# Optimization experiments

Measured on AMD Instinct MI355X. Metric: run time of the kernel, lower is better.

Reference implementation:

```python
import jax, jax.numpy as jnp
import numpy as np

B, T, N, F, CH = 64, 8, 2000, 16, 64  # batch, timesteps(=receptive field), nodes, in features, channels (h_dim//2)
TASK = CH          # task_dim = h_dim // 2
P_TREAT = 0.5      # args.p
P1 = 1.0           # args.p1
BN_EPS = 1e-5


def setup_inputs() -> dict:
    key = jax.random.key(0)
    ks = jax.random.split(key, 40)
    def rn(i, shape, s=0.1):
        return jax.random.normal(ks[i], shape, dtype=jnp.float32) * s
    return {
        "X": jax.random.normal(ks[0], (B, T, N, F), dtype=jnp.float32),
        "A": jax.random.uniform(ks[1], (N, N), dtype=jnp.float32),
        "C": jax.random.randint(ks[2], (B, N), 0, 2, dtype=jnp.int32),
        "Y": jax.random.uniform(ks[3], (B, N), dtype=jnp.float32),
        "Cc": jnp.zeros((B, N), jnp.float32),
        "start_w": rn(4, (CH, F)),
        "start_b": rn(5, (CH,), 0.01),
        "filt_w": rn(6, (3, CH, CH, 2)),
        "filt_b": rn(7, (3, CH), 0.01),
        "gate_w": rn(8, (3, CH, CH, 2)),
        "gate_b": rn(9, (3, CH), 0.01),
        "skip_w": rn(10, (3, CH, CH)),
        "skip_b": rn(11, (3, CH), 0.01),
        "bn_g": 1.0 + rn(12, (3, CH), 0.01),
        "bn_b": rn(13, (3, CH), 0.01),
        "nodevec1": jax.random.normal(ks[14], (N, 10), dtype=jnp.float32),
        "nodevec2": jax.random.normal(ks[15], (10, N), dtype=jnp.float32),
        "task_emb": rn(16, (TASK,)),
        "gcn_w": rn(17, (CH, 3 * CH)),
        "gcn_b": rn(18, (CH,), 0.01),
        "h0_w1": rn(19, (CH, TASK + CH)),
        "h0_b1": rn(20, (CH,), 0.01),
        "h0_w2": rn(21, (1, CH)),
        "h0_b2": rn(22, (1,), 0.01),
        "h1_w1": rn(23, (CH, TASK + CH)),
        "h1_b1": rn(24, (CH,), 0.01),
        "h1_w2": rn(25, (1, CH)),
        "h1_b2": rn(26, (1,), 0.01),
    }


def _conv1x1(x, w, b):
    # x: (B,Cin,N,L), w: (Cout,Cin)
    return jnp.einsum('bcnl,oc->bonl', x, w) + b[None, :, None, None]


def _dil_conv(x, w, b, d):
    # kernel (1,2), dilation d along time, no padding -> width shrinks by d
    L = x.shape[-1]
    y = (jnp.einsum('bcnl,oc->bonl', x[..., :L - d], w[:, :, 0])
         + jnp.einsum('bcnl,oc->bonl', x[..., d:], w[:, :, 1]))
    return y + b[None, :, None, None]


def reference(X, A, C, Y, Cc, start_w, start_b, filt_w, filt_b, gate_w, gate_b,
              skip_w, skip_b, bn_g, bn_b, nodevec1, nodevec2, task_emb, gcn_w, gcn_b,
              h0_w1, h0_b1, h0_w2, h0_b2, h1_w1, h1_b1, h1_w2, h1_b2):
    x = jnp.transpose(X, (0, 3, 2, 1))            # (B,F,N,T)
    x = _conv1x1(x, start_w, start_b)             # (B,CH,N,T)
    adp = jax.nn.softmax(jax.nn.relu(nodevec1 @ nodevec2), axis=1)  # (N,N)
    skip = None
    d = 1
    for i in range(3):  # layers, dilations 1,2,4
        res = x
        f = jnp.tanh(_dil_conv(res, filt_w[i], filt_b[i], d))
        g = jax.nn.sigmoid(_dil_conv(res, gate_w[i], gate_b[i], d))
        x = f * g
        s = _conv1x1(x, skip_w[i], skip_b[i])
        skip = s if skip is None else s + skip[..., -s.shape[-1]:]
        x = x + res[..., -x.shape[-1]:]
        # eval-mode BatchNorm2d with running_mean=0, running_var=1
        scale = (bn_g[i] / jnp.sqrt(1.0 + BN_EPS))[None, :, None, None]
        x = x * scale + bn_b[i][None, :, None, None]
        d *= 2
    # gcn on skip (width 1): out = [x, A@x, A@(A@x)] -> concat -> 1x1 (dropout=eval identity)
    x1 = jnp.einsum('bcvl,vw->bcwl', skip, adp)
    x2 = jnp.einsum('bcvl,vw->bcwl', x1, adp)
    h = jnp.concatenate([skip, x1, x2], axis=1)   # (B,3CH,N,1)
    gx = jax.nn.relu(_conv1x1(h, gcn_w, gcn_b))   # (B,CH,N,1)
    bs, _, n_nodes, _ = gx.shape
    task = jnp.broadcast_to(task_emb[None, :, None, None], (bs, TASK, n_nodes, 1))
    z = jnp.concatenate([task, gx], axis=1)       # (B,TASK+CH,N,1)

    def hyp(w1, b1, w2, b2):
        hh = jax.nn.relu(_conv1x1(z, w1, b1))
        return _conv1x1(hh, w2, b2).reshape(-1)

    y1 = jax.nn.sigmoid(hyp(h1_w1, h1_b1, h1_w2, h1_b2))
    y0 = jax.nn.sigmoid(hyp(h0_w1, h0_b1, h0_w2, h0_b2))
    t = C.reshape(-1)
    y = jnp.where(t > 0, y1, y0)
    yc = jnp.clip(y, 1e-7, 1.0 - 1e-7)
    Yf = Y.reshape(-1)
    bce = -jnp.mean(Yf * jnp.log(yc) + (1.0 - Yf) * jnp.log(1.0 - yc))
    # linear MMD (mmd2_lin, CFR): masked means, jit-friendly
    zb = jnp.transpose(z, (0, 2, 1, 3)).reshape(bs * n_nodes, -1)  # (B*N, TASK+CH)
    tm = (t > 0).astype(zb.dtype)
    mean_t = (tm @ zb) / jnp.maximum(tm.sum(), 1.0)
    mean_c = ((1.0 - tm) @ zb) / jnp.maximum((1.0 - tm).sum(), 1.0)
    imb = jnp.sum((2.0 * P_TREAT * mean_t - 2.0 * (1.0 - P_TREAT) * mean_c) ** 2)
    loss = bce + P1 * imb
    return (loss, y, y0, y1)
```

## Files before the change

kernel.cpp:

```cpp
#include <hip/hip_runtime.h>
#include <cstdint>

#define NB 64
#define TT 8
#define NN 2000
#define NF 16
#define NCH 64
#define NPAD 2048
#define BCD 4096
#define ITEMS 128000

#define OFF_ADPF  0
#define OFF_ST    4194304
#define OFF_X2    0
#define OFF_ADPT  8388608
#define OFF_S     10485760
#define OFF_X1F   18874368
#define OFF_X1T   27262976
#define OFF_C01   31457280
#define OFF_WGCNT (OFF_C01 + 128)
#define OFF_W1TT  (OFF_WGCNT + 12288)
#define OFF_PART  (OFF_W1TT + 8192)
#define OFF_RED   (OFF_PART + 270336)
#define OFF_WAW   (OFF_RED + 136)
#define OFF_SWW   (OFF_WAW + 24576)
#define OFF_WSTW  (OFF_SWW + 6144)

#define SWZK(k, x) (((k) & ~63) | (((((k) >> 3) & 7) ^ ((x) & 7)) << 3) | ((k) & 7))
#define GSWZ(n) ((((n) >> 3) ^ (n)) & 7)

typedef __attribute__((ext_vector_type(8))) short short8;
typedef __attribute__((ext_vector_type(4))) float f32x4;
typedef const __attribute__((address_space(1))) uint32_t* gas_t;
typedef __attribute__((address_space(3))) uint32_t* las_t;

__device__ __forceinline__ float fast_rcp(float x) { return __builtin_amdgcn_rcpf(x); }
__device__ __forceinline__ float fast_tanh(float x) {
    x = fminf(fmaxf(x, -10.f), 10.f);
    float e = __expf(2.f * x);
    return (e - 1.f) * fast_rcp(e + 1.f);
}
__device__ __forceinline__ float fast_sigmoid(float x) {
    return fast_rcp(1.f + __expf(-x));
}
__device__ __forceinline__ unsigned short f2bf(float f) {
    uint32_t u = __float_as_uint(f);
    u += 0x7fff + ((u >> 16) & 1);
    return (unsigned short)(u >> 16);
}
__device__ __forceinline__ float bf2f(unsigned short b) {
    return __uint_as_float(((uint32_t)b) << 16);
}

__global__ __launch_bounds__(256) void prep_kernel(const float* __restrict__ gcn_w,
                            const float* __restrict__ h0_w1, const float* __restrict__ h0_b1,
                            const float* __restrict__ h1_w1, const float* __restrict__ h1_b1,
                            const float* __restrict__ task_emb,
                            const float* __restrict__ filt_w, const float* __restrict__ gate_w,
                            const float* __restrict__ skip_w, const float* __restrict__ start_w,
                            float* __restrict__ c01, float* __restrict__ wgcnT,
                            float* __restrict__ w1tT,
                            unsigned short* __restrict__ waw,
                            unsigned short* __restrict__ sww,
                            unsigned short* __restrict__ wstw)
{
    const int GS = 64 * 256;
    int gt = blockIdx.x * 256 + threadIdx.x;
    for (int idx = gt; idx < 64 * 192; idx += GS) {
        int o = idx / 192, j = idx % 192;
        wgcnT[j * 64 + o] = gcn_w[idx];
    }
    for (int idx = gt; idx < 4096; idx += GS) {
        int o = idx >> 6, c = idx & 63;
        w1tT[c * 64 + o]        = h0_w1[o * 128 + 64 + c];
        w1tT[4096 + c * 64 + o] = h1_w1[o * 128 + 64 + c];
    }
    for (int job = gt; job < 3 * 2 * 128 * 8; job += GS) {
        int L = job / 2048, rem = job % 2048;
        int p = rem >> 10, rem2 = rem & 1023;
        int r = rem2 >> 3, chp = rem2 & 7;
        int cho = chp ^ (r & 7);
        #pragma unroll
        for (int i = 0; i < 8; ++i) {
            int c = cho * 8 + i;
            float v = (r < 64) ? filt_w[L * 8192 + r * 128 + c * 2 + p]
                               : gate_w[L * 8192 + (r - 64) * 128 + c * 2 + p];
            waw[((L * 2 + p) * 128 + r) * 64 + chp * 8 + i] = f2bf(v);
        }
    }
    for (int job = gt; job < 3 * 64 * 8; job += GS) {
        int L = job / 512, rem = job % 512;
        int r = rem >> 3, chp = rem & 7;
        int cho = chp ^ (r & 7);
        #pragma unroll
        for (int i = 0; i < 8; ++i)
            sww[(L * 64 + r) * 64 + chp * 8 + i] = f2bf(skip_w[L * 4096 + r * 64 + cho * 8 + i]);
    }
    for (int job = gt; job < 64 * 8; job += GS) {
        int r = job >> 3, chp = job & 7;
        int cho = chp ^ (r & 7);
        #pragma unroll
        for (int i = 0; i < 8; ++i) {
            int k = cho * 8 + i;
            wstw[r * 64 + chp * 8 + i] = (k < 16) ? f2bf(start_w[r * 16 + k]) : (unsigned short)0;
        }
    }
    if (gt < 128) {
        int head = gt >> 6, o = gt & 63;
        const float* w1 = head ? h1_w1 : h0_w1;
        const float* b1 = head ? h1_b1 : h0_b1;
        float a = b1[o];
        for (int k = 0; k < 64; ++k) a = fmaf(w1[o * 128 + k], task_emb[k], a);
        c01[gt] = a;
    }
}

__global__ __launch_bounds__(256) void adp_kernel(const float* __restrict__ nv1,
                                                  const float* __restrict__ nv2,
                                                  float* __restrict__ adpF)
{
    __shared__ float nv1s[10];
    __shared__ float rbuf[4];
    int tid = threadIdx.x;
    int r = blockIdx.x;
    if (tid < 10) nv1s[tid] = nv1[r * 10 + tid];
    __syncthreads();

    float val[8];
    float vmax = -3.4e38f;
    #pragma unroll
    for (int s = 0; s < 8; ++s) {
        int j = tid + s * 256;
        if (j < NN) {
            float v = 0.f;
            #pragma unroll
            for (int k = 0; k < 10; ++k) v = fmaf(nv1s[k], nv2[k * NN + j], v);
            v = fmaxf(v, 0.f);
            val[s] = v;
            vmax = fmaxf(vmax, v);
        } else val[s] = -3.4e38f;
    }
    for (int off = 32; off; off >>= 1) vmax = fmaxf(vmax, __shfl_down(vmax, off, 64));
    if ((tid & 63) == 0) rbuf[tid >> 6] = vmax;
    __syncthreads();
    vmax = fmaxf(fmaxf(rbuf[0], rbuf[1]), fmaxf(rbuf[2], rbuf[3]));
    __syncthreads();
    float sum = 0.f;
    #pragma unroll
    for (int s = 0; s < 8; ++s) {
        int j = tid + s * 256;
        if (j < NN) { val[s] = expf(val[s] - vmax); sum += val[s]; }
    }
    for (int off = 32; off; off >>= 1) sum += __shfl_down(sum, off, 64);
    if ((tid & 63) == 0) rbuf[tid >> 6] = sum;
    __syncthreads();
    sum = rbuf[0] + rbuf[1] + rbuf[2] + rbuf[3];
    float inv = 1.f / sum;
    #pragma unroll
    for (int s = 0; s < 8; ++s) {
        int j = tid + s * 256;
        if (j < NN) adpF[(size_t)r * NPAD + j] = val[s] * inv;
    }
}

__global__ __launch_bounds__(256) void transpose_adp(const float* __restrict__ adpF,
                                                     unsigned short* __restrict__ adpT)
{
    __shared__ float tile[64][65];
    int tid = threadIdx.x;
    int r0 = blockIdx.x * 64;
    int j0 = blockIdx.y * 64;
    #pragma unroll
    for (int s = 0; s < 16; ++s) {
        int idx = s * 256 + tid;
        int i = idx >> 6, jj = idx & 63;
        int r = r0 + i, j = j0 + jj;
        tile[i][jj] = (r < NN && j < NN) ? adpF[(size_t)r * NPAD + j] : 0.f;
    }
    __syncthreads();
    #pragma unroll
    for (int s = 0; s < 2; ++s) {
        int slot = s * 256 + tid;
        int j = slot >> 3, ch = slot & 7;
        short8 v;
        #pragma unroll
        for (int e = 0; e < 8; ++e) v[e] = (short)f2bf(tile[ch * 8 + e][j]);
        *(short8*)&adpT[(size_t)(j0 + j) * NPAD + r0 + ((ch ^ (j & 7)) << 3)] = v;
    }
}

template<int NG, int WOUT, int D>
__device__ __forceinline__ void mfma_phaseB(int L,
    const unsigned short* __restrict__ xb, unsigned short* __restrict__ gbuf,
    const unsigned short* __restrict__ WA, const float* __restrict__ biasAll,
    int wave, int lr, int lk)
{
    if (wave >= NG) return;
    int idx = wave * 16 + lr;
    int n = (idx / WOUT) * 8 + (idx % WOUT);
    f32x4 aF[4], aG[4];
    #pragma unroll
    for (int mt = 0; mt < 4; ++mt) {
        aF[mt] = (f32x4){0.f, 0.f, 0.f, 0.f};
        aG[mt] = (f32x4){0.f, 0.f, 0.f, 0.f};
    }
    #pragma unroll
    for (int p = 0; p < 2; ++p) {
        int nb = n + p * D;
        const unsigned short* WAp = WA + p * 8192;
        #pragma unroll
        for (int ks = 0; ks < 2; ++ks) {
            short8 bv = *(const short8*)&xb[(nb * 8 + ((ks * 4 + lk) ^ (nb & 7))) * 8];
            #pragma unroll
            for (int mt = 0; mt < 4; ++mt) {
                int r = mt * 16 + lr;
                short8 av = *(const short8*)&WAp[(r * 8 + ((ks * 4 + lk) ^ (r & 7))) * 8];
                aF[mt] = __builtin_amdgcn_mfma_f32_16x16x32_bf16(av, bv, aF[mt], 0, 0, 0);
            }
            #pragma unroll
            for (int mt = 0; mt < 4; ++mt) {
                int r = (mt + 4) * 16 + lr;
                short8 av = *(const short8*)&WAp[(r * 8 + ((ks * 4 + lk) ^ (r & 7))) * 8];
                aG[mt] = __builtin_amdgcn_mfma_f32_16x16x32_bf16(av, bv, aG[mt], 0, 0, 0);
            }
        }
    }
    int gs = GSWZ(n);
    #pragma unroll
    for (int mt = 0; mt < 4; ++mt) {
        int ob = mt * 16 + lk * 4;
        ushort4 p;
        p.x = f2bf(fast_tanh(aF[mt][0] + biasAll[L * 128 + ob + 0]) * fast_sigmoid(aG[mt][0] + biasAll[L * 128 + 64 + ob + 0]));
        p.y = f2bf(fast_tanh(aF[mt][1] + biasAll[L * 128 + ob + 1]) * fast_sigmoid(aG[mt][1] + biasAll[L * 128 + 64 + ob + 1]));
        p.z = f2bf(fast_tanh(aF[mt][2] + biasAll[L * 128 + ob + 2]) * fast_sigmoid(aG[mt][2] + biasAll[L * 128 + 64 + ob + 2]));
        p.w = f2bf(fast_tanh(aF[mt][3] + biasAll[L * 128 + ob + 3]) * fast_sigmoid(aG[mt][3] + biasAll[L * 128 + 64 + ob + 3]));
        *(ushort4*)&gbuf[((n * 8) + ((mt * 2 + (lk >> 1)) ^ gs)) * 8 + (lk & 1) * 4] = p;
    }
}

template<int L, int D, int WOUT>
__device__ __forceinline__ void phaseC_conv(unsigned short* __restrict__ xb,
    const unsigned short* __restrict__ gbuf,
    const float* __restrict__ bn_g, const float* __restrict__ bn_b,
    float xreg[8], int wave, int o)
{
    float bsc = bn_g[L * 64 + o] * rsqrtf(1.0f + 1e-5f);
    float bsh = bn_b[L * 64 + o];
    int g = wave;
    #pragma unroll
    for (int t = 0; t < WOUT; ++t) {
        int n = g * 8 + t;
        float gv = bf2f(gbuf[(n * 8 + ((o >> 3) ^ GSWZ(n))) * 8 + (o & 7)]);
        float nx = (gv + xreg[t + D]) * bsc + bsh;
        xreg[t] = nx;
        xb[(n * 8 + ((o >> 3) ^ (n & 7))) * 8 + (o & 7)] = f2bf(nx);
    }
}

__device__ __forceinline__ void phaseC_skip(int LASTT,
    const unsigned short* __restrict__ gbuf, const unsigned short* __restrict__ SW,
    f32x4 skacc[4], int wave, int lr, int lk)
{
    if (wave != 0) return;
    int n = lr * 8 + LASTT;
    int gs = GSWZ(n);
    #pragma unroll
    for (int ks = 0; ks < 2; ++ks) {
        short8 bv = *(const short8*)&gbuf[(n * 8 + ((ks * 4 + lk) ^ gs)) * 8];
        #pragma unroll
        for (int mt = 0; mt < 4; ++mt) {
            int r = mt * 16 + lr;
            short8 av = *(const short8*)&SW[(r * 8 + ((ks * 4 + lk) ^ (r & 7))) * 8];
            skacc[mt] = __builtin_amdgcn_mfma_f32_16x16x32_bf16(av, bv, skacc[mt], 0, 0, 0);
        }
    }
}

__global__ __launch_bounds__(1024) void temporal_kernel(
    const float* __restrict__ X,
    const float* __restrict__ start_b,
    const unsigned short* __restrict__ waw,
    const unsigned short* __restrict__ sww,
    const unsigned short* __restrict__ wstw,
    const float* __restrict__ filt_b, const float* __restrict__ gate_b,
    const float* __restrict__ skip_b,
    const float* __restrict__ bn_g, const float* __restrict__ bn_b,
    float* __restrict__ S, unsigned short* __restrict__ St)
{
    extern __shared__ float smem[];
    unsigned short* xb   = (unsigned short*)smem;
    unsigned short* gbuf = (unsigned short*)(smem + 4096);
    unsigned short* WA   = (unsigned short*)(smem + 8192);
    unsigned short* SW   = (unsigned short*)(smem + 16384);
    float* biasAll       = smem + 18432;

    int tid = threadIdx.x;
    int wave = tid >> 6, lane = tid & 63;
    int lr = lane & 15, lk = lane >> 4;
    int o = lane;
    int item0 = blockIdx.x * 16;

    if (tid < 512)
        __builtin_amdgcn_global_load_lds((gas_t)(wstw + tid * 8), (las_t)(WA + tid * 8), 16, 0, 0);
    if (tid < 384) {
        int L = tid >> 7, oo = tid & 127;
        biasAll[tid] = (oo < 64) ? filt_b[L * 64 + oo] : gate_b[L * 64 + oo - 64];
    }
    {
        int n = tid >> 3, c = tid & 7;
        int g = n >> 3, t = n & 7;
        int ig = item0 + g, b = ig / NN, nn = ig - b * NN;
        int cho = c ^ (n & 7);
        short8 v = {0, 0, 0, 0, 0, 0, 0, 0};
        if (cho < 2) {
            const float* src = &X[((size_t)(b * TT + t) * NN + nn) * NF + cho * 8];
            float4 f0 = *(const float4*)src;
            float4 f1 = *(const float4*)(src + 4);
            v[0] = (short)f2bf(f0.x); v[1] = (short)f2bf(f0.y);
            v[2] = (short)f2bf(f0.z); v[3] = (short)f2bf(f0.w);
            v[4] = (short)f2bf(f1.x); v[5] = (short)f2bf(f1.y);
            v[6] = (short)f2bf(f1.z); v[7] = (short)f2bf(f1.w);
        }
        *(short8*)&xb[(n * 8 + c) * 8] = v;
    }
    __syncthreads();

    if (wave < 8) {
        f32x4 aS[4];
        #pragma unroll
        for (int mt = 0; mt < 4; ++mt) aS[mt] = (f32x4){0.f, 0.f, 0.f, 0.f};
        int n = wave * 16 + lr;
        short8 bv = *(const short8*)&xb[(n * 8 + (lk ^ (n & 7))) * 8];
        #pragma unroll
        for (int mt = 0; mt < 4; ++mt) {
            int r = mt * 16 + lr;
            short8 av = *(const short8*)&WA[(r * 8 + (lk ^ (r & 7))) * 8];
            aS[mt] = __builtin_amdgcn_mfma_f32_16x16x32_bf16(av, bv, aS[mt], 0, 0, 0);
        }
        int gs = GSWZ(n);
        #pragma unroll
        for (int mt = 0; mt < 4; ++mt) {
            ushort4 p;
            p.x = f2bf(aS[mt][0]); p.y = f2bf(aS[mt][1]);
            p.z = f2bf(aS[mt][2]); p.w = f2bf(aS[mt][3]);
            *(ushort4*)&gbuf[((n * 8) + ((mt * 2 + (lk >> 1)) ^ gs)) * 8 + (lk & 1) * 4] = p;
        }
    }
    if (tid < 512)
        __builtin_amdgcn_global_load_lds((gas_t)(sww + tid * 8), (las_t)(SW + tid * 8), 16, 0, 0);
    __syncthreads();

    float xreg[8];
    f32x4 skacc[4];
    #pragma unroll
    for (int mt = 0; mt < 4; ++mt) skacc[mt] = (f32x4){0.f, 0.f, 0.f, 0.f};

    {
        __builtin_amdgcn_global_load_lds((gas_t)(waw + (size_t)tid * 8),
                                         (las_t)(WA + tid * 8), 16, 0, 0);
        __builtin_amdgcn_global_load_lds((gas_t)(waw + (size_t)(tid + 1024) * 8),
                                         (las_t)(WA + (tid + 1024) * 8), 16, 0, 0);
        float sb = start_b[o];
        int g = wave;
        #pragma unroll
        for (int t = 0; t < 8; ++t) {
            int n = g * 8 + t;
            float gv = bf2f(gbuf[(n * 8 + ((o >> 3) ^ GSWZ(n))) * 8 + (o & 7)]) + sb;
            xreg[t] = gv;
            xb[(n * 8 + ((o >> 3) ^ (n & 7))) * 8 + (o & 7)] = f2bf(gv);
        }
    }
    __syncthreads();

    mfma_phaseB<7, 7, 1>(0, xb, gbuf, WA, biasAll, wave, lr, lk);
    __syncthreads();
    phaseC_skip(6, gbuf, SW, skacc, wave, lr, lk);
    phaseC_conv<0, 1, 7>(xb, gbuf, bn_g, bn_b, xreg, wave, o);
    __builtin_amdgcn_global_load_lds((gas_t)(waw + (size_t)(16384 + tid * 8)),
                                     (las_t)(WA + tid * 8), 16, 0, 0);
    __builtin_amdgcn_global_load_lds((gas_t)(waw + (size_t)(16384 + (tid + 1024) * 8)),
                                     (las_t)(WA + (tid + 1024) * 8), 16, 0, 0);
    __syncthreads();

    mfma_phaseB<5, 5, 2>(1, xb, gbuf, WA, biasAll, wave, lr, lk);
    if (tid < 512)
        __builtin_amdgcn_global_load_lds((gas_t)(sww + (size_t)(4096 + tid * 8)),
                                         (las_t)(SW + tid * 8), 16, 0, 0);
    __syncthreads();
    phaseC_skip(4, gbuf, SW, skacc, wave, lr, lk);
    phaseC_conv<1, 2, 5>(xb, gbuf, bn_g, bn_b, xreg, wave, o);
    __builtin_amdgcn_global_load_lds((gas_t)(waw + (size_t)(32768 + tid * 8)),
                                     (las_t)(WA + tid * 8), 16, 0, 0);
    __builtin_amdgcn_global_load_lds((gas_t)(waw + (size_t)(32768 + (tid + 1024) * 8)),
                                     (las_t)(WA + (tid + 1024) * 8), 16, 0, 0);
    __syncthreads();

    mfma_phaseB<1, 1, 4>(2, xb, gbuf, WA, biasAll, wave, lr, lk);
    if (tid < 512)
        __builtin_amdgcn_global_load_lds((gas_t)(sww + (size_t)(8192 + tid * 8)),
                                         (las_t)(SW + tid * 8), 16, 0, 0);
    __syncthreads();
    phaseC_skip(0, gbuf, SW, skacc, wave, lr, lk);

    if (wave == 0) {
        int ig = item0 + lr, b = ig / NN, nn = ig - b * NN;
        #pragma unroll
        for (int mt = 0; mt < 4; ++mt) {
            #pragma unroll
            for (int j = 0; j < 4; ++j) {
                int oo = mt * 16 + lk * 4 + j;
                float v = skacc[mt][j] + skip_b[oo] + skip_b[64 + oo] + skip_b[128 + oo];
                int bc = b * 64 + oo;
                S[(size_t)nn * BCD + bc] = v;
                St[(size_t)bc * NPAD + SWZK(nn, oo)] = f2bf(v);
            }
        }
    }
}

__global__ __launch_bounds__(256) void gemm_mfma(
    const unsigned short* __restrict__ A, const unsigned short* __restrict__ B,
    float* __restrict__ Cf, unsigned short* __restrict__ Ct)
{
    __shared__ unsigned short As[128 * 64];
    __shared__ unsigned short Bs[128 * 64];
    int tid = threadIdx.x;
    int wave = tid >> 6, lane = tid & 63;
    int lk = lane >> 4, lr = lane & 15;
    int n0 = blockIdx.x * 128, m0 = blockIdx.y * 128;
    int wm = wave >> 1, wn = wave & 1;

    f32x4 acc[4][4];
    #pragma unroll
    for (int i = 0; i < 4; ++i)
        #pragma unroll
        for (int j = 0; j < 4; ++j)
            acc[i][j] = (f32x4){0.f, 0.f, 0.f, 0.f};

    for (int k0 = 0; k0 < NPAD; k0 += 64) {
        #pragma unroll
        for (int i = 0; i < 4; ++i) {
            int chunk = wave * 4 + i;
            int row = chunk * 8 + (lane >> 3);
            int koff = (lane & 7) * 8;
            __builtin_amdgcn_global_load_lds(
                (gas_t)(A + (size_t)(m0 + row) * NPAD + k0 + koff),
                (las_t)(&As[chunk * 512]), 16, 0, 0);
            __builtin_amdgcn_global_load_lds(
                (gas_t)(B + (size_t)(n0 + row) * NPAD + k0 + koff),
                (las_t)(&Bs[chunk * 512]), 16, 0, 0);
        }
        __syncthreads();
        #pragma unroll
        for (int s = 0; s < 2; ++s) {
            short8 av[4], bv[4];
            #pragma unroll
            for (int f = 0; f < 4; ++f) {
                int m = wm * 64 + f * 16 + lr;
                int ca = ((s * 4 + lk) ^ (m & 7));
                av[f] = *(const short8*)&As[m * 64 + ca * 8];
                int n = wn * 64 + f * 16 + lr;
                int cb = ((s * 4 + lk) ^ (n & 7));
                bv[f] = *(const short8*)&Bs[n * 64 + cb * 8];
            }
            #pragma unroll
            for (int fi = 0; fi < 4; ++fi)
                #pragma unroll
                for (int fj = 0; fj < 4; ++fj)
                    acc[fi][fj] = __builtin_amdgcn_mfma_f32_16x16x32_bf16(
                        av[fi], bv[fj], acc[fi][fj], 0, 0, 0);
        }
        __syncthreads();
    }

    #pragma unroll
    for (int fi = 0; fi < 4; ++fi) {
        #pragma unroll
        for (int fj = 0; fj < 4; ++fj) {
            int m = m0 + wm * 64 + fi * 16 + lk * 4;
            int n = n0 + wn * 64 + fj * 16 + lr;
            f32x4 v = acc[fi][fj];
            if (Cf) {
                Cf[(size_t)(m + 0) * BCD + n] = v[0];
                Cf[(size_t)(m + 1) * BCD + n] = v[1];
                Cf[(size_t)(m + 2) * BCD + n] = v[2];
                Cf[(size_t)(m + 3) * BCD + n] = v[3];
            }
            if (Ct) {
                ushort4 p;
                p.x = f2bf(v[0]); p.y = f2bf(v[1]);
                p.z = f2bf(v[2]); p.w = f2bf(v[3]);
                *(ushort4*)&Ct[(size_t)n * NPAD + SWZK(m, n)] = p;
            }
        }
    }
}

__global__ __launch_bounds__(256) void head_kernel(
    const float* __restrict__ S, const float* __restrict__ x1f,
    const float* __restrict__ x2,
    const float* __restrict__ wgcnT, const float* __restrict__ gcn_b,
    const float* __restrict__ c01, const float* __restrict__ w1tT,
    const float* __restrict__ h0_w2, const float* __restrict__ h0_b2,
    const float* __restrict__ h1_w2, const float* __restrict__ h1_b2,
    const int* __restrict__ Ct, const float* __restrict__ Yf,
    float* __restrict__ out, float* __restrict__ partials)
{
    __shared__ float hl[4][4][192];
    __shared__ float gxl[4][4][64];
    int tid = threadIdx.x;
    int wave = tid >> 6, o = tid & 63;
    int wid = blockIdx.x * 4 + wave;
    float w2a = h0_w2[o], w2b = h1_w2[o];
    float b20 = h0_b2[0], b21 = h1_b2[0];
    float cb = gcn_b[o], c0a = c01[o], c0b = c01[64 + o];

    float accT = 0.f, accC = 0.f, bce = 0.f, cT = 0.f, cC = 0.f;

    for (int base = wid * 4; base < ITEMS; base += 2048 * 4) {
        #pragma unroll
        for (int it = 0; it < 4; ++it) {
            int item = base + it;
            int b = item / NN, n = item - b * NN;
            int bc = b * 64 + o;
            hl[wave][it][o]       = S[(size_t)n * BCD + bc];
            hl[wave][it][64 + o]  = x1f[(size_t)n * BCD + bc];
            hl[wave][it][128 + o] = x2[(size_t)n * BCD + bc];
        }
        float a0 = cb, a1 = cb, a2 = cb, a3 = cb;
        for (int j = 0; j < 192; ++j) {
            float w = wgcnT[j * 64 + o];
            a0 = fmaf(w, hl[wave][0][j], a0);
            a1 = fmaf(w, hl[wave][1][j], a1);
            a2 = fmaf(w, hl[wave][2][j], a2);
            a3 = fmaf(w, hl[wave][3][j], a3);
        }
        float gxv[4] = {fmaxf(a0, 0.f), fmaxf(a1, 0.f), fmaxf(a2, 0.f), fmaxf(a3, 0.f)};
        #pragma unroll
        for (int it = 0; it < 4; ++it) gxl[wave][it][o] = gxv[it];

        float p0[4], p1[4];
        #pragma unroll
        for (int it = 0; it < 4; ++it) { p0[it] = c0a; p1[it] = c0b; }
        for (int c = 0; c < 64; ++c) {
            float w0 = w1tT[c * 64 + o];
            float w1 = w1tT[4096 + c * 64 + o];
            float g0 = gxl[wave][0][c], g1 = gxl[wave][1][c];
            float g2 = gxl[wave][2][c], g3 = gxl[wave][3][c];
            p0[0] = fmaf(w0, g0, p0[0]); p0[1] = fmaf(w0, g1, p0[1]);
            p0[2] = fmaf(w0, g2, p0[2]); p0[3] = fmaf(w0, g3, p0[3]);
            p1[0] = fmaf(w1, g0, p1[0]); p1[1] = fmaf(w1, g1, p1[1]);
            p1[2] = fmaf(w1, g2, p1[2]); p1[3] = fmaf(w1, g3, p1[3]);
        }
        #pragma unroll
        for (int it = 0; it < 4; ++it) {
            float r0 = w2a * fmaxf(p0[it], 0.f);
            float r1 = w2b * fmaxf(p1[it], 0.f);
            #pragma unroll
            for (int off = 32; off; off >>= 1) {
                r0 += __shfl_down(r0, off, 64);
                r1 += __shfl_down(r1, off, 64);
            }
            int item = base + it;
            int tt = Ct[item];
            if (o == 0) {
                float y0 = 1.f / (1.f + expf(-(r0 + b20)));
                float y1 = 1.f / (1.f + expf(-(r1 + b21)));
                float y = (tt > 0) ? y1 : y0;
                out[1 + item] = y;
                out[1 + ITEMS + item] = y0;
                out[1 + 2 * ITEMS + item] = y1;
                float yc = fminf(fmaxf(y, 1e-7f), 1.f - 1e-7f);
                float Yv = Yf[item];
                bce -= Yv * logf(yc) + (1.f - Yv) * logf(1.f - yc);
                if (tt > 0) cT += 1.f; else cC += 1.f;
            }
            if (tt > 0) accT += gxv[it]; else accC += gxv[it];
        }
    }
    partials[wid * 132 + o] = accT;
    partials[wid * 132 + 64 + o] = accC;
    if (o == 0) {
        partials[wid * 132 + 128] = bce;
        partials[wid * 132 + 129] = cT;
        partials[wid * 132 + 130] = cC;
    }
}

__global__ __launch_bounds__(256) void reduce_kernel(const float* __restrict__ partials,
                                                     float* __restrict__ red)
{
    __shared__ float rb[4];
    int slot = blockIdx.x;
    int tid = threadIdx.x;
    float s = 0.f;
    for (int w = tid; w < 2048; w += 256) s += partials[w * 132 + slot];
    #pragma unroll
    for (int off = 32; off; off >>= 1) s += __shfl_down(s, off, 64);
    if ((tid & 63) == 0) rb[tid >> 6] = s;
    __syncthreads();
    if (tid == 0) red[slot] = rb[0] + rb[1] + rb[2] + rb[3];
}

__global__ void final_kernel(const float* __restrict__ red,
                             const float* __restrict__ task_emb,
                             float* __restrict__ out)
{
    int tid = threadIdx.x;
    float cT = red[129], cC = red[130];
    float iT = 1.f / fmaxf(cT, 1.f), iC = 1.f / fmaxf(cC, 1.f);
    float d1 = task_emb[tid] * (cT * iT) - task_emb[tid] * (cC * iC);
    float d2 = red[tid] * iT - red[64 + tid] * iC;
    float p = d1 * d1 + d2 * d2;
    #pragma unroll
    for (int off = 32; off; off >>= 1) p += __shfl_down(p, off, 64);
    if (tid == 0) out[0] = red[128] * (1.f / (float)ITEMS) + p;
}

extern "C" void kernel_launch(void* const* d_in, const int* in_sizes, int n_in,
                              void* d_out, int out_size, void* d_ws, size_t ws_size,
                              hipStream_t stream)
{
    const float* X       = (const float*)d_in[0];
    const int*   Ct      = (const int*)d_in[2];
    const float* Yf      = (const float*)d_in[3];
    const float* start_w = (const float*)d_in[5];
    const float* start_b = (const float*)d_in[6];
    const float* filt_w  = (const float*)d_in[7];
    const float* filt_b  = (const float*)d_in[8];
    const float* gate_w  = (const float*)d_in[9];
    const float* gate_b  = (const float*)d_in[10];
    const float* skip_w  = (const float*)d_in[11];
    const float* skip_b  = (const float*)d_in[12];
    const float* bn_g    = (const float*)d_in[13];
    const float* bn_b    = (const float*)d_in[14];
    const float* nv1     = (const float*)d_in[15];
    const float* nv2     = (const float*)d_in[16];
    const float* task    = (const float*)d_in[17];
    const float* gcn_w   = (const float*)d_in[18];
    const float* gcn_b   = (const float*)d_in[19];
    const float* h0_w1   = (const float*)d_in[20];
    const float* h0_b1   = (const float*)d_in[21];
    const float* h0_w2   = (const float*)d_in[22];
    const float* h0_b2   = (const float*)d_in[23];
    const float* h1_w1   = (const float*)d_in[24];
    const float* h1_b1   = (const float*)d_in[25];
    const float* h1_w2   = (const float*)d_in[26];
    const float* h1_b2   = (const float*)d_in[27];

    float* ws    = (float*)d_ws;
    float* adpF  = ws + OFF_ADPF;
    unsigned short* St   = (unsigned short*)(ws + OFF_ST);
    float* x2    = ws + OFF_X2;
    unsigned short* adpT = (unsigned short*)(ws + OFF_ADPT);
    float* S     = ws + OFF_S;
    float* x1f   = ws + OFF_X1F;
    unsigned short* x1t  = (unsigned short*)(ws + OFF_X1T);
    float* c01   = ws + OFF_C01;
    float* wgcnT = ws + OFF_WGCNT;
    float* w1tT  = ws + OFF_W1TT;
    float* part  = ws + OFF_PART;
    float* red   = ws + OFF_RED;
    unsigned short* waw  = (unsigned short*)(ws + OFF_WAW);
    unsigned short* sww  = (unsigned short*)(ws + OFF_SWW);
    unsigned short* wstw = (unsigned short*)(ws + OFF_WSTW);
    float* outp  = (float*)d_out;

    hipMemsetAsync(St, 0, (size_t)BCD * NPAD * sizeof(unsigned short), stream);

    prep_kernel<<<64, 256, 0, stream>>>(gcn_w, h0_w1, h0_b1, h1_w1, h1_b1, task,
                                        filt_w, gate_w, skip_w, start_w,
                                        c01, wgcnT, w1tT, waw, sww, wstw);
    adp_kernel<<<NN, 256, 0, stream>>>(nv1, nv2, adpF);
    dim3 tg(NPAD / 64, NPAD / 64);
    transpose_adp<<<tg, 256, 0, stream>>>(adpF, adpT);

    const int K2_LDS = 18816 * 4;
    hipFuncSetAttribute(reinterpret_cast<const void*>(temporal_kernel),
                        hipFuncAttributeMaxDynamicSharedMemorySize, K2_LDS);
    temporal_kernel<<<ITEMS / 16, 1024, K2_LDS, stream>>>(
        X, start_b, waw, sww, wstw, filt_b, gate_b,
        skip_b, bn_g, bn_b, S, St);

    dim3 gg(BCD / 128, NPAD / 128);
    gemm_mfma<<<gg, 256, 0, stream>>>(adpT, St, x1f, x1t);
    gemm_mfma<<<gg, 256, 0, stream>>>(adpT, x1t, x2, nullptr);

    head_kernel<<<512, 256, 0, stream>>>(S, x1f, x2, wgcnT, gcn_b, c01, w1tT,
                                         h0_w2, h0_b2, h1_w2, h1_b2,
                                         Ct, Yf, outp, part);
    reduce_kernel<<<131, 256, 0, stream>>>(part, red);
    final_kernel<<<1, 64, 0, stream>>>(red, task, outp);
}
```

Baseline: 629.1 us.

## Double temporal kernel items per block and swizzle GEMM block order

The temporal kernel now processes 32 node-items per 1024-thread block instead of 16. Each wave handles two item groups, the skip MFMA uses two waves, and the LDS buffers are enlarged to match. This amortises the per-block weight loads into LDS and the barrier costs over twice the work, at the price of more LDS per block and possibly lower occupancy. Separately, the GEMM launches as a 1D grid with a remapped block index so that consecutive blocks share rows of the adjacency matrix, aiming to improve L2 reuse.

```diff
diff --git a/kernel.cpp b/kernel.cpp
--- a/kernel.cpp
+++ b/kernel.cpp
@@ -242,18 +242,21 @@
 __device__ __forceinline__ void phaseC_conv(unsigned short* __restrict__ xb,
     const unsigned short* __restrict__ gbuf,
     const float* __restrict__ bn_g, const float* __restrict__ bn_b,
-    float xreg[8], int wave, int o)
+    float xreg[2][8], int wave, int o)
 {
     float bsc = bn_g[L * 64 + o] * rsqrtf(1.0f + 1e-5f);
     float bsh = bn_b[L * 64 + o];
-    int g = wave;
-    #pragma unroll
-    for (int t = 0; t < WOUT; ++t) {
-        int n = g * 8 + t;
-        float gv = bf2f(gbuf[(n * 8 + ((o >> 3) ^ GSWZ(n))) * 8 + (o & 7)]);
-        float nx = (gv + xreg[t + D]) * bsc + bsh;
-        xreg[t] = nx;
-        xb[(n * 8 + ((o >> 3) ^ (n & 7))) * 8 + (o & 7)] = f2bf(nx);
+    #pragma unroll
+    for (int gi = 0; gi < 2; ++gi) {
+        int g = wave * 2 + gi;
+        #pragma unroll
+        for (int t = 0; t < WOUT; ++t) {
+            int n = g * 8 + t;
+            float gv = bf2f(gbuf[(n * 8 + ((o >> 3) ^ GSWZ(n))) * 8 + (o & 7)]);
+            float nx = (gv + xreg[gi][t + D]) * bsc + bsh;
+            xreg[gi][t] = nx;
+            xb[(n * 8 + ((o >> 3) ^ (n & 7))) * 8 + (o & 7)] = f2bf(nx);
+        }
     }
 }
 
@@ -261,8 +264,9 @@
     const unsigned short* __restrict__ gbuf, const unsigned short* __restrict__ SW,
     f32x4 skacc[4], int wave, int lr, int lk)
 {
-    if (wave != 0) return;
-    int n = lr * 8 + LASTT;
+    if (wave >= 2) return;
+    int g = wave * 16 + lr;
+    int n = g * 8 + LASTT;
     int gs = GSWZ(n);
     #pragma unroll
     for (int ks = 0; ks < 2; ++ks) {
@@ -289,16 +293,16 @@
 {
     extern __shared__ float smem[];
     unsigned short* xb   = (unsigned short*)smem;
-    unsigned short* gbuf = (unsigned short*)(smem + 4096);
-    unsigned short* WA   = (unsigned short*)(smem + 8192);
-    unsigned short* SW   = (unsigned short*)(smem + 16384);
-    float* biasAll       = smem + 18432;
+    unsigned short* gbuf = (unsigned short*)(smem + 8192);
+    unsigned short* WA   = (unsigned short*)(smem + 16384);
+    unsigned short* SW   = (unsigned short*)(smem + 24576);
+    float* biasAll       = smem + 26624;
 
     int tid = threadIdx.x;
     int wave = tid >> 6, lane = tid & 63;
     int lr = lane & 15, lk = lane >> 4;
     int o = lane;
-    int item0 = blockIdx.x * 16;
+    int item0 = blockIdx.x * 32;
 
     if (tid < 512)
         __builtin_amdgcn_global_load_lds((gas_t)(wstw + tid * 8), (las_t)(WA + tid * 8), 16, 0, 0);
@@ -306,8 +310,10 @@
         int L = tid >> 7, oo = tid & 127;
         biasAll[tid] = (oo < 64) ? filt_b[L * 64 + oo] : gate_b[L * 64 + oo - 64];
     }
-    {
-        int n = tid >> 3, c = tid & 7;
+    #pragma unroll
+    for (int s = 0; s < 2; ++s) {
+        int idx = s * 1024 + tid;
+        int n = idx >> 3, c = idx & 7;
         int g = n >> 3, t = n & 7;
         int ig = item0 + g, b = ig / NN, nn = ig - b * NN;
         int cho = c ^ (n & 7);
@@ -325,7 +331,7 @@
     }
     __syncthreads();
 
-    if (wave < 8) {
+    {
         f32x4 aS[4];
         #pragma unroll
         for (int mt = 0; mt < 4; ++mt) aS[mt] = (f32x4){0.f, 0.f, 0.f, 0.f};
@@ -350,7 +356,7 @@
         __builtin_amdgcn_global_load_lds((gas_t)(sww + tid * 8), (las_t)(SW + tid * 8), 16, 0, 0);
     __syncthreads();
 
-    float xreg[8];
+    float xreg[2][8];
     f32x4 skacc[4];
     #pragma unroll
     for (int mt = 0; mt < 4; ++mt) skacc[mt] = (f32x4){0.f, 0.f, 0.f, 0.f};
@@ -361,18 +367,21 @@
         __builtin_amdgcn_global_load_lds((gas_t)(waw + (size_t)(tid + 1024) * 8),
                                          (las_t)(WA + (tid + 1024) * 8), 16, 0, 0);
         float sb = start_b[o];
-        int g = wave;
-        #pragma unroll
-        for (int t = 0; t < 8; ++t) {
-            int n = g * 8 + t;
-            float gv = bf2f(gbuf[(n * 8 + ((o >> 3) ^ GSWZ(n))) * 8 + (o & 7)]) + sb;
-            xreg[t] = gv;
-            xb[(n * 8 + ((o >> 3) ^ (n & 7))) * 8 + (o & 7)] = f2bf(gv);
-        }
-    }
-    __syncthreads();
-
-    mfma_phaseB<7, 7, 1>(0, xb, gbuf, WA, biasAll, wave, lr, lk);
+        #pragma unroll
+        for (int gi = 0; gi < 2; ++gi) {
+            int g = wave * 2 + gi;
+            #pragma unroll
+            for (int t = 0; t < 8; ++t) {
+                int n = g * 8 + t;
+                float gv = bf2f(gbuf[(n * 8 + ((o >> 3) ^ GSWZ(n))) * 8 + (o & 7)]) + sb;
+                xreg[gi][t] = gv;
+                xb[(n * 8 + ((o >> 3) ^ (n & 7))) * 8 + (o & 7)] = f2bf(gv);
+            }
+        }
+    }
+    __syncthreads();
+
+    mfma_phaseB<14, 7, 1>(0, xb, gbuf, WA, biasAll, wave, lr, lk);
     __syncthreads();
     phaseC_skip(6, gbuf, SW, skacc, wave, lr, lk);
     phaseC_conv<0, 1, 7>(xb, gbuf, bn_g, bn_b, xreg, wave, o);
@@ -382,7 +391,7 @@
                                      (las_t)(WA + (tid + 1024) * 8), 16, 0, 0);
     __syncthreads();
 
-    mfma_phaseB<5, 5, 2>(1, xb, gbuf, WA, biasAll, wave, lr, lk);
+    mfma_phaseB<10, 5, 2>(1, xb, gbuf, WA, biasAll, wave, lr, lk);
     if (tid < 512)
         __builtin_amdgcn_global_load_lds((gas_t)(sww + (size_t)(4096 + tid * 8)),
                                          (las_t)(SW + tid * 8), 16, 0, 0);
@@ -395,15 +404,16 @@
                                      (las_t)(WA + (tid + 1024) * 8), 16, 0, 0);
     __syncthreads();
 
-    mfma_phaseB<1, 1, 4>(2, xb, gbuf, WA, biasAll, wave, lr, lk);
+    mfma_phaseB<2, 1, 4>(2, xb, gbuf, WA, biasAll, wave, lr, lk);
     if (tid < 512)
         __builtin_amdgcn_global_load_lds((gas_t)(sww + (size_t)(8192 + tid * 8)),
                                          (las_t)(SW + tid * 8), 16, 0, 0);
     __syncthreads();
     phaseC_skip(0, gbuf, SW, skacc, wave, lr, lk);
 
-    if (wave == 0) {
-        int ig = item0 + lr, b = ig / NN, nn = ig - b * NN;
+    if (wave < 2) {
+        int g = wave * 16 + lr;
+        int ig = item0 + g, b = ig / NN, nn = ig - b * NN;
         #pragma unroll
         for (int mt = 0; mt < 4; ++mt) {
             #pragma unroll
@@ -427,7 +437,10 @@
     int tid = threadIdx.x;
     int wave = tid >> 6, lane = tid & 63;
     int lk = lane >> 4, lr = lane & 15;
-    int n0 = blockIdx.x * 128, m0 = blockIdx.y * 128;
+    int lid = blockIdx.x;
+    int lid2 = (lid & 7) * 64 + (lid >> 3);
+    int bx = lid2 & 31, by = lid2 >> 5;
+    int n0 = bx * 128, m0 = by * 128;
     int wm = wave >> 1, wn = wave & 1;
 
     f32x4 acc[4][4];
@@ -675,16 +688,15 @@
     dim3 tg(NPAD / 64, NPAD / 64);
     transpose_adp<<<tg, 256, 0, stream>>>(adpF, adpT);
 
-    const int K2_LDS = 18816 * 4;
+    const int K2_LDS = 27008 * 4;
     hipFuncSetAttribute(reinterpret_cast<const void*>(temporal_kernel),
                         hipFuncAttributeMaxDynamicSharedMemorySize, K2_LDS);
-    temporal_kernel<<<ITEMS / 16, 1024, K2_LDS, stream>>>(
+    temporal_kernel<<<ITEMS / 32, 1024, K2_LDS, stream>>>(
         X, start_b, waw, sww, wstw, filt_b, gate_b,
         skip_b, bn_g, bn_b, S, St);
 
-    dim3 gg(BCD / 128, NPAD / 128);
-    gemm_mfma<<<gg, 256, 0, stream>>>(adpT, St, x1f, x1t);
-    gemm_mfma<<<gg, 256, 0, stream>>>(adpT, x1t, x2, nullptr);
+    gemm_mfma<<<512, 256, 0, stream>>>(adpT, St, x1f, x1t);
+    gemm_mfma<<<512, 256, 0, stream>>>(adpT, x1t, x2, nullptr);
 
     head_kernel<<<512, 256, 0, stream>>>(S, x1f, x2, wgcnT, gcn_b, c01, w1tT,
                                          h0_w2, h0_b2, h1_w2, h1_b2,
```

Measured after the change: 544.0 us. 13.5% less time.
